# Kernel optimization log

Hardware: AMD Instinct MI355X
Metric: run time of the kernel (lower is better)

## Reference

```python
import jax, jax.numpy as jnp
import numpy as np

B, S, D, H = 2, 2048, 1024, 16
HD = D // H
NEG = -1000000.0


def setup_inputs() -> dict:
    key = jax.random.key(0)
    ks = jax.random.split(key, 8)
    sc = 1.0 / np.sqrt(D)
    return {
        "q": jax.random.normal(ks[0], (B, S, D), dtype=jnp.float32),
        "k": jax.random.normal(ks[1], (B, S, D), dtype=jnp.float32),
        "v": jax.random.normal(ks[2], (B, S, D), dtype=jnp.float32),
        "valid_lens": jax.random.randint(ks[3], (B,), 1, S + 1, dtype=jnp.int32),
        "Wq": jax.random.normal(ks[4], (D, D), dtype=jnp.float32) * sc,
        "Wk": jax.random.normal(ks[5], (D, D), dtype=jnp.float32) * sc,
        "Wv": jax.random.normal(ks[6], (D, D), dtype=jnp.float32) * sc,
        "Wo": jax.random.normal(ks[7], (D, D), dtype=jnp.float32) * sc,
    }


def reference(q, k, v, valid_lens, Wq, Wk, Wv, Wo):
    # projections: [B,S,D] -> [B,H,S,HD]
    def split_heads(x):
        return x.reshape(B, S, H, HD).transpose(0, 2, 1, 3)

    qh = split_heads(q @ Wq)
    kh = split_heads(k @ Wk)
    vh = split_heads(v @ Wv)

    # scaled dot-product scores: [B,H,Sq,Sk]
    scores = jnp.einsum("bhqd,bhkd->bhqk", qh, kh) / jnp.sqrt(
        jnp.asarray(HD, dtype=jnp.float32))

    # sequence mask over key axis: positions >= valid_len replaced by -1e6
    key_pos = jnp.arange(S, dtype=jnp.int32)
    mask = key_pos[None, :] < valid_lens[:, None]            # [B,Sk]
    scores = jnp.where(mask[:, None, None, :], scores, NEG)

    attn = jax.nn.softmax(scores, axis=-1)                   # dropout rate 0
    ctx = jnp.einsum("bhqk,bhkd->bhqd", attn, vh)            # [B,H,S,HD]
    out = ctx.transpose(0, 2, 1, 3).reshape(B, S, D)
    return out @ Wo
```

## Files before the change

### kernel.cpp

```cpp
#include <hip/hip_runtime.h>
#include <math.h>

#define NB 2
#define NS 2048
#define ND 1024
#define NH 16
#define NHD 64
#define GK 1024
#define NEG -1000000.0f

typedef __attribute__((ext_vector_type(4))) float f32x4;
typedef __attribute__((ext_vector_type(8))) _Float16 f16x8;
typedef __attribute__((ext_vector_type(4))) _Float16 f16x4;

typedef const __attribute__((address_space(1))) unsigned int* gas_t;
typedef __attribute__((address_space(3))) unsigned int* las_t;

__global__ __launch_bounds__(256) void wt_kernel(const float* __restrict__ Wq,
                                                 const float* __restrict__ Wk,
                                                 const float* __restrict__ Wv,
                                                 const float* __restrict__ Wo,
                                                 _Float16* __restrict__ WtBase) {
  __shared__ _Float16 Ts[64][72];
  const int which = blockIdx.x >> 8;
  const int rem = blockIdx.x & 255;
  const int tk = rem >> 4;
  const int tn = rem & 15;
  const float* W = which == 0 ? Wq : which == 1 ? Wk : which == 2 ? Wv : Wo;
  _Float16* Wt = WtBase + (size_t)which * (GK * ND);
  const int t = threadIdx.x;
#pragma unroll
  for (int p = 0; p < 4; ++p) {
    const int kr = (p << 4) + (t >> 4);
    const int nc = (t & 15) << 2;
    float4 v = *(const float4*)(W + (size_t)((tk << 6) + kr) * ND + (tn << 6) + nc);
    f16x4 h = {(_Float16)v.x, (_Float16)v.y, (_Float16)v.z, (_Float16)v.w};
    *(f16x4*)&Ts[kr][nc] = h;
  }
  __syncthreads();
#pragma unroll
  for (int p = 0; p < 4; ++p) {
    const int nr = (p << 4) + (t >> 4);
    const int kc = (t & 15) << 2;
    f16x4 h;
#pragma unroll
    for (int u = 0; u < 4; ++u) h[u] = Ts[kc + u][nr];
    *(f16x4*)(Wt + (size_t)((tn << 6) + nr) * GK + (tk << 6) + kc) = h;
  }
}

__global__ __launch_bounds__(256) void proj_kernel(const float* __restrict__ xq,
                                                   const float* __restrict__ xk,
                                                   const float* __restrict__ xv,
                                                   const _Float16* __restrict__ WtBase,
                                                   _Float16* __restrict__ Qh,
                                                   _Float16* __restrict__ Kh,
                                                   _Float16* __restrict__ VhT) {
  constexpr int BK = 32;
  __shared__ alignas(16) _Float16 As[128 * BK];
  __shared__ alignas(16) _Float16 Bs[128 * BK];

  int idx = ((blockIdx.x % 96) << 3) + (blockIdx.x / 96);
  const int which = idx >> 8;
  idx &= 255;
  const int bm = (idx >> 3) << 7;
  const int bn = (idx & 7) << 7;
  const float* A = which == 0 ? xq : which == 1 ? xk : xv;
  const _Float16* Bt = WtBase + (size_t)which * (ND * GK);

  const int tid = threadIdx.x, lane = tid & 63, w = tid >> 6;
  const int i16 = lane & 15, g4 = lane >> 4;
  const int wr = w >> 1, wc = w & 1;

  f32x4 acc[4][4] = {};

  for (int kt = 0; kt < GK / BK; ++kt) {
#pragma unroll
    for (int u = 0; u < 2; ++u) {
      const int c = (((w << 1) + u) << 6) + lane;
      const int r = c >> 2, sl = c & 3;
      const float* src = A + (size_t)(bm + r) * GK + (kt << 5) + ((sl ^ (r & 3)) << 3);
      float4 v0 = *(const float4*)src;
      float4 v1 = *(const float4*)(src + 4);
      f16x8 h;
#pragma unroll
      for (int j = 0; j < 4; ++j) { h[j] = (_Float16)v0[j]; h[4 + j] = (_Float16)v1[j]; }
      *(f16x8*)&As[(r << 5) + (sl << 3)] = h;
    }
#pragma unroll
    for (int u = 0; u < 2; ++u) {
      const int cb = ((w << 1) + u) << 6;
      const int c = cb + lane;
      const int r = c >> 2, sl = c & 3;
      __builtin_amdgcn_global_load_lds(
          (gas_t)(const void*)(Bt + (size_t)(bn + r) * GK + (kt << 5) + ((sl ^ (r & 3)) << 3)),
          (las_t)(void*)&Bs[cb << 3], 16, 0, 0);
    }
    __syncthreads();

    f16x8 af[4], bf[4];
#pragma unroll
    for (int mi = 0; mi < 4; ++mi) {
      const int r = (wr << 6) + (mi << 4) + i16;
      af[mi] = *(const f16x8*)&As[(r << 5) + ((g4 ^ (r & 3)) << 3)];
    }
#pragma unroll
    for (int ni = 0; ni < 4; ++ni) {
      const int r = (wc << 6) + (ni << 4) + i16;
      bf[ni] = *(const f16x8*)&Bs[(r << 5) + ((g4 ^ (r & 3)) << 3)];
    }
#pragma unroll
    for (int mi = 0; mi < 4; ++mi)
#pragma unroll
      for (int ni = 0; ni < 4; ++ni)
        acc[mi][ni] = __builtin_amdgcn_mfma_f32_16x16x32_f16(af[mi], bf[ni], acc[mi][ni], 0, 0, 0);
    __syncthreads();
  }

  if (which == 2) {
#pragma unroll
    for (int mi = 0; mi < 4; ++mi)
#pragma unroll
      for (int ni = 0; ni < 4; ++ni) {
        const int row0 = bm + (wr << 6) + (mi << 4) + (g4 << 2);
        const int col = bn + (wc << 6) + (ni << 4) + i16;
        const int bb = row0 >> 11, ss = row0 & (NS - 1);
        const int hh = col >> 6, dd = col & 63;
        f16x4 hv;
#pragma unroll
        for (int j = 0; j < 4; ++j) hv[j] = (_Float16)acc[mi][ni][j];
        *(f16x4*)&VhT[(((size_t)(bb * NH + hh) * NHD + dd) << 11) + ss] = hv;
      }
  } else {
    const float scale = which == 0 ? 0.125f : 1.0f;
    _Float16* Out = which == 0 ? Qh : Kh;
#pragma unroll
    for (int mi = 0; mi < 4; ++mi)
#pragma unroll
      for (int ni = 0; ni < 4; ++ni)
#pragma unroll
        for (int j = 0; j < 4; ++j) {
          const int row = bm + (wr << 6) + (mi << 4) + (g4 << 2) + j;
          const int col = bn + (wc << 6) + (ni << 4) + i16;
          const int bb = row >> 11, ss = row & (NS - 1);
          const int hh = col >> 6, dd = col & 63;
          Out[(((size_t)(bb * NH + hh) * NS + ss) << 6) + dd] = (_Float16)(acc[mi][ni][j] * scale);
        }
  }
}

__global__ __launch_bounds__(256) void attn_kernel(_Float16* __restrict__ Qc,
                                                   const _Float16* __restrict__ Kh,
                                                   const _Float16* __restrict__ VhT,
                                                   const int* __restrict__ valid_lens) {
  __shared__ alignas(16) _Float16 Ks[2][4096];
  __shared__ alignas(16) _Float16 Vt[2][4096];
  __shared__ alignas(16) _Float16 Ps[64][72];

  const int b0 = blockIdx.x;
  const int idx = ((b0 & 7) << 5) + ((b0 >> 8) << 8) + ((b0 >> 3) & 31);
  const int bh = idx >> 5, qt = idx & 31;
  const int valid = valid_lens[bh >> 4];
  const int tid = threadIdx.x, lane = tid & 63, w = tid >> 6;
  const int i16 = lane & 15, g4 = lane >> 4;

  _Float16* Qb = Qc + ((size_t)bh * NS + (qt << 6)) * NHD;
  const _Float16* Kb = Kh + (size_t)bh * NS * NHD;
  const _Float16* Vb = VhT + (size_t)bh * NHD * NS;

  f16x8 qf[2];
#pragma unroll
  for (int dc = 0; dc < 2; ++dc)
    qf[dc] = *(const f16x8*)(Qb + (size_t)((w << 4) + i16) * NHD + (dc << 5) + (g4 << 3));

  f32x4 acc[4] = {};
  float mrow[4] = {-1e30f, -1e30f, -1e30f, -1e30f};
  float lsum[4] = {0.f, 0.f, 0.f, 0.f};

  auto STAGE = [&](int buf, int t) {
#pragma unroll
    for (int u = 0; u < 2; ++u) {
      const int cb = ((w << 1) + u) << 6;
      const int c = cb + lane;
      const int r = c >> 3, sl = c & 7;
      const int so = (sl ^ (r & 7)) << 3;
      __builtin_amdgcn_global_load_lds(
          (gas_t)(const void*)(Kb + (size_t)((t << 6) + r) * NHD + so),
          (las_t)(void*)&Ks[buf][cb << 3], 16, 0, 0);
      __builtin_amdgcn_global_load_lds(
          (gas_t)(const void*)(Vb + (size_t)r * NS + (t << 6) + so),
          (las_t)(void*)&Vt[buf][cb << 3], 16, 0, 0);
    }
  };

  const int ntiles = (valid + 63) >> 6;
  STAGE(0, 0);

  for (int t = 0; t < ntiles; ++t) {
    __syncthreads();
    if (t + 1 < ntiles) STAGE((t + 1) & 1, t + 1);
    const int buf = t & 1;
    const bool full = ((t + 1) << 6) <= valid;

    float pj[4][4];
#pragma unroll
    for (int cf = 0; cf < 4; ++cf) {
      f32x4 sa = {};
      const int r = (cf << 4) + i16;
#pragma unroll
      for (int dc = 0; dc < 2; ++dc) {
        f16x8 kf = *(const f16x8*)&Ks[buf][(r << 6) + ((((dc << 2) + g4) ^ (r & 7)) << 3)];
        sa = __builtin_amdgcn_mfma_f32_16x16x32_f16(qf[dc], kf, sa, 0, 0, 0);
      }
      if (full) {
#pragma unroll
        for (int j = 0; j < 4; ++j) pj[cf][j] = sa[j];
      } else {
        const int kvcol = (t << 6) + r;
#pragma unroll
        for (int j = 0; j < 4; ++j) pj[cf][j] = (kvcol >= valid) ? NEG : sa[j];
      }
    }

    float tmax[4];
#pragma unroll
    for (int j = 0; j < 4; ++j)
      tmax[j] = fmaxf(fmaxf(pj[0][j], pj[1][j]), fmaxf(pj[2][j], pj[3][j]));
    for (int off = 1; off < 16; off <<= 1)
#pragma unroll
      for (int j = 0; j < 4; ++j)
        tmax[j] = fmaxf(tmax[j], __shfl_xor(tmax[j], off, 64));

    float rowsum[4] = {0.f, 0.f, 0.f, 0.f};
#pragma unroll
    for (int j = 0; j < 4; ++j) {
      const float mn = fmaxf(mrow[j], tmax[j]);
      const float scv = __expf(mrow[j] - mn);
      mrow[j] = mn;
      lsum[j] *= scv;
#pragma unroll
      for (int dn = 0; dn < 4; ++dn) acc[dn][j] *= scv;
    }
#pragma unroll
    for (int cf = 0; cf < 4; ++cf)
#pragma unroll
      for (int j = 0; j < 4; ++j) {
        const float p = __expf(pj[cf][j] - mrow[j]);
        rowsum[j] += p;
        Ps[(w << 4) + (g4 << 2) + j][(cf << 4) + i16] = (_Float16)p;
      }
    for (int off = 1; off < 16; off <<= 1)
#pragma unroll
      for (int j = 0; j < 4; ++j)
        rowsum[j] += __shfl_xor(rowsum[j], off, 64);
#pragma unroll
    for (int j = 0; j < 4; ++j) lsum[j] += rowsum[j];

#pragma unroll
    for (int ks = 0; ks < 2; ++ks) {
      f16x8 pf = *(const f16x8*)&Ps[(w << 4) + i16][(ks << 5) + (g4 << 3)];
#pragma unroll
      for (int dn = 0; dn < 4; ++dn) {
        const int d = (dn << 4) + i16;
        f16x8 vf = *(const f16x8*)&Vt[buf][(d << 6) + ((((ks << 2) + g4) ^ (d & 7)) << 3)];
        acc[dn] = __builtin_amdgcn_mfma_f32_16x16x32_f16(pf, vf, acc[dn], 0, 0, 0);
      }
    }
  }

#pragma unroll
  for (int dn = 0; dn < 4; ++dn)
#pragma unroll
    for (int j = 0; j < 4; ++j) {
      const int qrow = (w << 4) + (g4 << 2) + j;
      Qb[(size_t)qrow * NHD + (dn << 4) + i16] = (_Float16)(acc[dn][j] / lsum[j]);
    }
}

__global__ __launch_bounds__(256) void out_kernel(const _Float16* __restrict__ ctx,
                                                  const _Float16* __restrict__ Wot,
                                                  float* __restrict__ Out) {
  constexpr int BK = 32;
  __shared__ alignas(16) _Float16 As[128 * BK];
  __shared__ alignas(16) _Float16 Bs[64 * BK];

  const int idx = ((blockIdx.x % 64) << 3) + (blockIdx.x / 64);
  const int bm = (idx >> 4) << 7;
  const int bn = (idx & 15) << 6;

  const int tid = threadIdx.x, lane = tid & 63, w = tid >> 6;
  const int i16 = lane & 15, g4 = lane >> 4;
  const int wr = w >> 1, wc = w & 1;

  f32x4 acc[4][2] = {};

  for (int kt = 0; kt < GK / BK; ++kt) {
#pragma unroll
    for (int u = 0; u < 2; ++u) {
      const int cb = ((w << 1) + u) << 6;
      const int c = cb + lane;
      const int r = c >> 2, sl = c & 3;
      const int m = bm + r;
      const int kcol = (kt << 5) + ((sl ^ (r & 3)) << 3);
      const int bb = m >> 11, ss = m & (NS - 1);
      const int hh = kcol >> 6, dd = kcol & 63;
      __builtin_amdgcn_global_load_lds(
          (gas_t)(const void*)(ctx + (((size_t)(bb * NH + hh) * NS + ss) << 6) + dd),
          (las_t)(void*)&As[cb << 3], 16, 0, 0);
    }
    {
      const int cb = w << 6;
      const int c = cb + lane;
      const int r = c >> 2, sl = c & 3;
      __builtin_amdgcn_global_load_lds(
          (gas_t)(const void*)(Wot + (size_t)(bn + r) * GK + (kt << 5) + ((sl ^ (r & 3)) << 3)),
          (las_t)(void*)&Bs[cb << 3], 16, 0, 0);
    }
    __syncthreads();

    f16x8 af[4], bf[2];
#pragma unroll
    for (int mi = 0; mi < 4; ++mi) {
      const int r = (wr << 6) + (mi << 4) + i16;
      af[mi] = *(const f16x8*)&As[(r << 5) + ((g4 ^ (r & 3)) << 3)];
    }
#pragma unroll
    for (int ni = 0; ni < 2; ++ni) {
      const int r = (wc << 5) + (ni << 4) + i16;
      bf[ni] = *(const f16x8*)&Bs[(r << 5) + ((g4 ^ (r & 3)) << 3)];
    }
#pragma unroll
    for (int mi = 0; mi < 4; ++mi)
#pragma unroll
      for (int ni = 0; ni < 2; ++ni)
        acc[mi][ni] = __builtin_amdgcn_mfma_f32_16x16x32_f16(af[mi], bf[ni], acc[mi][ni], 0, 0, 0);
    __syncthreads();
  }

#pragma unroll
  for (int mi = 0; mi < 4; ++mi)
#pragma unroll
    for (int ni = 0; ni < 2; ++ni)
#pragma unroll
      for (int j = 0; j < 4; ++j) {
        const int row = bm + (wr << 6) + (mi << 4) + (g4 << 2) + j;
        const int col = bn + (wc << 5) + (ni << 4) + i16;
        Out[(size_t)row * ND + col] = acc[mi][ni][j];
      }
}

extern "C" void kernel_launch(void* const* d_in, const int* in_sizes, int n_in,
                              void* d_out, int out_size, void* d_ws, size_t ws_size,
                              hipStream_t stream) {
  const float* q  = (const float*)d_in[0];
  const float* k  = (const float*)d_in[1];
  const float* v  = (const float*)d_in[2];
  const int*   vl = (const int*)d_in[3];
  const float* Wq = (const float*)d_in[4];
  const float* Wk = (const float*)d_in[5];
  const float* Wv = (const float*)d_in[6];
  const float* Wo = (const float*)d_in[7];

  _Float16* ws = (_Float16*)d_ws;
  _Float16* Qh  = ws;
  _Float16* Kh  = ws + 4194304;
  _Float16* VhT = ws + 8388608;
  _Float16* Wt  = ws + 12582912;

  wt_kernel<<<dim3(1024), dim3(256), 0, stream>>>(Wq, Wk, Wv, Wo, Wt);
  proj_kernel<<<dim3(768), dim3(256), 0, stream>>>(q, k, v, Wt, Qh, Kh, VhT);
  attn_kernel<<<dim3(NB * NH * (NS >> 6)), dim3(256), 0, stream>>>(Qh, Kh, VhT, vl);
  out_kernel<<<dim3(512), dim3(256), 0, stream>>>(Qh, Wt + 3145728, (float*)d_out);
}
```

Measured before the change: 226.1 us.

## Pre-convert activations to fp16, split projection GEMMs, and streamline attention softmax

```diff
diff --git a/kernel.cpp b/kernel.cpp
--- a/kernel.cpp
+++ b/kernel.cpp
@@ -12,136 +12,162 @@
 typedef __attribute__((ext_vector_type(4))) float f32x4;
 typedef __attribute__((ext_vector_type(8))) _Float16 f16x8;
 typedef __attribute__((ext_vector_type(4))) _Float16 f16x4;
+typedef __attribute__((ext_vector_type(2))) __fp16 fp16x2_t;
 
 typedef const __attribute__((address_space(1))) unsigned int* gas_t;
 typedef __attribute__((address_space(3))) unsigned int* las_t;
 
-__global__ __launch_bounds__(256) void wt_kernel(const float* __restrict__ Wq,
-                                                 const float* __restrict__ Wk,
-                                                 const float* __restrict__ Wv,
-                                                 const float* __restrict__ Wo,
-                                                 _Float16* __restrict__ WtBase) {
-  __shared__ _Float16 Ts[64][72];
-  const int which = blockIdx.x >> 8;
-  const int rem = blockIdx.x & 255;
-  const int tk = rem >> 4;
-  const int tn = rem & 15;
-  const float* W = which == 0 ? Wq : which == 1 ? Wk : which == 2 ? Wv : Wo;
-  _Float16* Wt = WtBase + (size_t)which * (GK * ND);
-  const int t = threadIdx.x;
-#pragma unroll
-  for (int p = 0; p < 4; ++p) {
-    const int kr = (p << 4) + (t >> 4);
-    const int nc = (t & 15) << 2;
-    float4 v = *(const float4*)(W + (size_t)((tk << 6) + kr) * ND + (tn << 6) + nc);
-    f16x4 h = {(_Float16)v.x, (_Float16)v.y, (_Float16)v.z, (_Float16)v.w};
-    *(f16x4*)&Ts[kr][nc] = h;
-  }
-  __syncthreads();
-#pragma unroll
-  for (int p = 0; p < 4; ++p) {
-    const int nr = (p << 4) + (t >> 4);
-    const int kc = (t & 15) << 2;
-    f16x4 h;
-#pragma unroll
-    for (int u = 0; u < 4; ++u) h[u] = Ts[kc + u][nr];
-    *(f16x4*)(Wt + (size_t)((tn << 6) + nr) * GK + (tk << 6) + kc) = h;
-  }
-}
-
-__global__ __launch_bounds__(256) void proj_kernel(const float* __restrict__ xq,
+__global__ __launch_bounds__(256) void prep_kernel(const float* __restrict__ Wq,
+                                                   const float* __restrict__ Wk,
+                                                   const float* __restrict__ Wv,
+                                                   const float* __restrict__ Wo,
+                                                   const float* __restrict__ xq,
                                                    const float* __restrict__ xk,
                                                    const float* __restrict__ xv,
-                                                   const _Float16* __restrict__ WtBase,
-                                                   _Float16* __restrict__ Qh,
-                                                   _Float16* __restrict__ Kh,
-                                                   _Float16* __restrict__ VhT) {
-  constexpr int BK = 32;
-  __shared__ alignas(16) _Float16 As[128 * BK];
-  __shared__ alignas(16) _Float16 Bs[128 * BK];
-
-  int idx = ((blockIdx.x % 96) << 3) + (blockIdx.x / 96);
-  const int which = idx >> 8;
-  idx &= 255;
-  const int bm = (idx >> 3) << 7;
-  const int bn = (idx & 7) << 7;
-  const float* A = which == 0 ? xq : which == 1 ? xk : xv;
-  const _Float16* Bt = WtBase + (size_t)which * (ND * GK);
+                                                   _Float16* __restrict__ WtBase,
+                                                   _Float16* __restrict__ xhq,
+                                                   _Float16* __restrict__ xhk,
+                                                   _Float16* __restrict__ xhv) {
+  const int t = threadIdx.x;
+  if (blockIdx.x < 1024) {
+    __shared__ _Float16 Ts[64][72];
+    const int which = blockIdx.x >> 8;
+    const int rem = blockIdx.x & 255;
+    const int tk = rem >> 4;
+    const int tn = rem & 15;
+    const float* W = which == 0 ? Wq : which == 1 ? Wk : which == 2 ? Wv : Wo;
+    _Float16* Wt = WtBase + (size_t)which * (GK * ND);
+#pragma unroll
+    for (int p = 0; p < 4; ++p) {
+      const int kr = (p << 4) + (t >> 4);
+      const int nc = (t & 15) << 2;
+      float4 v = *(const float4*)(W + (size_t)((tk << 6) + kr) * ND + (tn << 6) + nc);
+      f16x4 h = {(_Float16)v.x, (_Float16)v.y, (_Float16)v.z, (_Float16)v.w};
+      *(f16x4*)&Ts[kr][nc] = h;
+    }
+    __syncthreads();
+#pragma unroll
+    for (int p = 0; p < 4; ++p) {
+      const int nr = (p << 4) + (t >> 4);
+      const int kc = (t & 15) << 2;
+      f16x4 h;
+#pragma unroll
+      for (int u = 0; u < 4; ++u) h[u] = Ts[kc + u][nr];
+      *(f16x4*)(Wt + (size_t)((tn << 6) + nr) * GK + (tk << 6) + kc) = h;
+    }
+  } else {
+    const int cid = blockIdx.x - 1024;
+    const int which = cid >> 11;
+    const float* src = which == 0 ? xq : which == 1 ? xk : xv;
+    _Float16* dst = which == 0 ? xhq : which == 1 ? xhk : xhv;
+    const size_t e0 = ((((size_t)(cid & 2047)) << 8) + t) << 3;
+    float4 v0 = *(const float4*)(src + e0);
+    float4 v1 = *(const float4*)(src + e0 + 4);
+    f16x8 h;
+#pragma unroll
+    for (int j = 0; j < 4; ++j) { h[j] = (_Float16)(&v0.x)[j]; h[4 + j] = (_Float16)(&v1.x)[j]; }
+    *(f16x8*)(dst + e0) = h;
+  }
+}
+
+template<int MODE>
+__global__ __launch_bounds__(256) void gemm16_kernel(const _Float16* __restrict__ A0,
+                                                     const _Float16* __restrict__ A1,
+                                                     const _Float16* __restrict__ Bt0,
+                                                     _Float16* __restrict__ O0,
+                                                     _Float16* __restrict__ O1) {
+  constexpr int BN = (MODE == 0) ? 128 : 64;
+  constexpr int NF = BN / 32;
+  __shared__ alignas(16) _Float16 As[128 * 32];
+  __shared__ alignas(16) _Float16 Bs[BN * 32];
+
+  const int b = blockIdx.x;
+  const int wg = ((b & 7) << 6) + (b >> 3);
+  int which, bm, bn;
+  if (MODE == 0) {
+    which = wg >> 8;
+    const int rem = wg & 255;
+    bm = (rem >> 3) << 7;
+    bn = (rem & 7) << 7;
+  } else {
+    which = 0;
+    bm = (wg >> 4) << 7;
+    bn = (wg & 15) << 6;
+  }
+  const _Float16* A = (MODE == 0 && which == 1) ? A1 : A0;
+  const _Float16* Bt = Bt0 + (size_t)which * (ND * GK);
 
   const int tid = threadIdx.x, lane = tid & 63, w = tid >> 6;
   const int i16 = lane & 15, g4 = lane >> 4;
   const int wr = w >> 1, wc = w & 1;
 
-  f32x4 acc[4][4] = {};
-
-  for (int kt = 0; kt < GK / BK; ++kt) {
-#pragma unroll
-    for (int u = 0; u < 2; ++u) {
-      const int c = (((w << 1) + u) << 6) + lane;
-      const int r = c >> 2, sl = c & 3;
-      const float* src = A + (size_t)(bm + r) * GK + (kt << 5) + ((sl ^ (r & 3)) << 3);
-      float4 v0 = *(const float4*)src;
-      float4 v1 = *(const float4*)(src + 4);
-      f16x8 h;
-#pragma unroll
-      for (int j = 0; j < 4; ++j) { h[j] = (_Float16)v0[j]; h[4 + j] = (_Float16)v1[j]; }
-      *(f16x8*)&As[(r << 5) + (sl << 3)] = h;
-    }
+  f32x4 acc[4][NF] = {};
+
+  for (int kt = 0; kt < GK / 32; ++kt) {
 #pragma unroll
     for (int u = 0; u < 2; ++u) {
       const int cb = ((w << 1) + u) << 6;
       const int c = cb + lane;
       const int r = c >> 2, sl = c & 3;
       __builtin_amdgcn_global_load_lds(
+          (gas_t)(const void*)(A + (size_t)(bm + r) * GK + (kt << 5) + ((sl ^ (r & 3)) << 3)),
+          (las_t)(void*)&As[cb << 3], 16, 0, 0);
+    }
+#pragma unroll
+    for (int u = 0; u < BN / 64; ++u) {
+      const int cb = ((w * (BN / 64)) + u) << 6;
+      const int c = cb + lane;
+      const int r = c >> 2, sl = c & 3;
+      __builtin_amdgcn_global_load_lds(
           (gas_t)(const void*)(Bt + (size_t)(bn + r) * GK + (kt << 5) + ((sl ^ (r & 3)) << 3)),
           (las_t)(void*)&Bs[cb << 3], 16, 0, 0);
     }
     __syncthreads();
 
-    f16x8 af[4], bf[4];
+    f16x8 af[4], bf[NF];
 #pragma unroll
     for (int mi = 0; mi < 4; ++mi) {
       const int r = (wr << 6) + (mi << 4) + i16;
       af[mi] = *(const f16x8*)&As[(r << 5) + ((g4 ^ (r & 3)) << 3)];
     }
 #pragma unroll
-    for (int ni = 0; ni < 4; ++ni) {
-      const int r = (wc << 6) + (ni << 4) + i16;
+    for (int ni = 0; ni < NF; ++ni) {
+      const int r = wc * (BN / 2) + (ni << 4) + i16;
       bf[ni] = *(const f16x8*)&Bs[(r << 5) + ((g4 ^ (r & 3)) << 3)];
     }
 #pragma unroll
     for (int mi = 0; mi < 4; ++mi)
 #pragma unroll
-      for (int ni = 0; ni < 4; ++ni)
+      for (int ni = 0; ni < NF; ++ni)
         acc[mi][ni] = __builtin_amdgcn_mfma_f32_16x16x32_f16(af[mi], bf[ni], acc[mi][ni], 0, 0, 0);
     __syncthreads();
   }
 
-  if (which == 2) {
+  if (MODE == 1) {
 #pragma unroll
     for (int mi = 0; mi < 4; ++mi)
 #pragma unroll
-      for (int ni = 0; ni < 4; ++ni) {
+      for (int ni = 0; ni < NF; ++ni) {
         const int row0 = bm + (wr << 6) + (mi << 4) + (g4 << 2);
-        const int col = bn + (wc << 6) + (ni << 4) + i16;
+        const int col = bn + wc * (BN / 2) + (ni << 4) + i16;
         const int bb = row0 >> 11, ss = row0 & (NS - 1);
         const int hh = col >> 6, dd = col & 63;
         f16x4 hv;
 #pragma unroll
         for (int j = 0; j < 4; ++j) hv[j] = (_Float16)acc[mi][ni][j];
-        *(f16x4*)&VhT[(((size_t)(bb * NH + hh) * NHD + dd) << 11) + ss] = hv;
+        *(f16x4*)&O0[(((size_t)(bb * NH + hh) * NHD + dd) << 11) + ss] = hv;
       }
   } else {
-    const float scale = which == 0 ? 0.125f : 1.0f;
-    _Float16* Out = which == 0 ? Qh : Kh;
+    const float scale = (which == 0) ? 0.125f : 1.0f;
+    _Float16* Out = (which == 0) ? O0 : O1;
 #pragma unroll
     for (int mi = 0; mi < 4; ++mi)
 #pragma unroll
-      for (int ni = 0; ni < 4; ++ni)
+      for (int ni = 0; ni < NF; ++ni)
 #pragma unroll
         for (int j = 0; j < 4; ++j) {
           const int row = bm + (wr << 6) + (mi << 4) + (g4 << 2) + j;
-          const int col = bn + (wc << 6) + (ni << 4) + i16;
+          const int col = bn + wc * (BN / 2) + (ni << 4) + i16;
           const int bb = row >> 11, ss = row & (NS - 1);
           const int hh = col >> 6, dd = col & 63;
           Out[(((size_t)(bb * NH + hh) * NS + ss) << 6) + dd] = (_Float16)(acc[mi][ni][j] * scale);
@@ -155,7 +181,7 @@
                                                    const int* __restrict__ valid_lens) {
   __shared__ alignas(16) _Float16 Ks[2][4096];
   __shared__ alignas(16) _Float16 Vt[2][4096];
-  __shared__ alignas(16) _Float16 Ps[64][72];
+  __shared__ alignas(16) unsigned int PsW[2048];
 
   const int b0 = blockIdx.x;
   const int idx = ((b0 & 7) << 5) + ((b0 >> 8) << 8) + ((b0 >> 3) & 31);
@@ -163,6 +189,7 @@
   const int valid = valid_lens[bh >> 4];
   const int tid = threadIdx.x, lane = tid & 63, w = tid >> 6;
   const int i16 = lane & 15, g4 = lane >> 4;
+  const int qrow = (w << 4) + i16;
 
   _Float16* Qb = Qc + ((size_t)bh * NS + (qt << 6)) * NHD;
   const _Float16* Kb = Kh + (size_t)bh * NS * NHD;
@@ -171,11 +198,11 @@
   f16x8 qf[2];
 #pragma unroll
   for (int dc = 0; dc < 2; ++dc)
-    qf[dc] = *(const f16x8*)(Qb + (size_t)((w << 4) + i16) * NHD + (dc << 5) + (g4 << 3));
+    qf[dc] = *(const f16x8*)(Qb + (size_t)qrow * NHD + (dc << 5) + (g4 << 3));
 
   f32x4 acc[4] = {};
-  float mrow[4] = {-1e30f, -1e30f, -1e30f, -1e30f};
-  float lsum[4] = {0.f, 0.f, 0.f, 0.f};
+  float mrow = -1e30f;
+  float lsum = 0.f;
 
   auto STAGE = [&](int buf, int t) {
 #pragma unroll
@@ -210,55 +237,63 @@
 #pragma unroll
       for (int dc = 0; dc < 2; ++dc) {
         f16x8 kf = *(const f16x8*)&Ks[buf][(r << 6) + ((((dc << 2) + g4) ^ (r & 7)) << 3)];
-        sa = __builtin_amdgcn_mfma_f32_16x16x32_f16(qf[dc], kf, sa, 0, 0, 0);
+        sa = __builtin_amdgcn_mfma_f32_16x16x32_f16(kf, qf[dc], sa, 0, 0, 0);
       }
       if (full) {
 #pragma unroll
         for (int j = 0; j < 4; ++j) pj[cf][j] = sa[j];
       } else {
-        const int kvcol = (t << 6) + r;
-#pragma unroll
-        for (int j = 0; j < 4; ++j) pj[cf][j] = (kvcol >= valid) ? NEG : sa[j];
-      }
-    }
-
-    float tmax[4];
-#pragma unroll
-    for (int j = 0; j < 4; ++j)
-      tmax[j] = fmaxf(fmaxf(pj[0][j], pj[1][j]), fmaxf(pj[2][j], pj[3][j]));
-    for (int off = 1; off < 16; off <<= 1)
-#pragma unroll
-      for (int j = 0; j < 4; ++j)
-        tmax[j] = fmaxf(tmax[j], __shfl_xor(tmax[j], off, 64));
-
-    float rowsum[4] = {0.f, 0.f, 0.f, 0.f};
-#pragma unroll
-    for (int j = 0; j < 4; ++j) {
-      const float mn = fmaxf(mrow[j], tmax[j]);
-      const float scv = __expf(mrow[j] - mn);
-      mrow[j] = mn;
-      lsum[j] *= scv;
-#pragma unroll
-      for (int dn = 0; dn < 4; ++dn) acc[dn][j] *= scv;
-    }
+        const int kvb = (t << 6) + (cf << 4) + (g4 << 2);
+#pragma unroll
+        for (int j = 0; j < 4; ++j) pj[cf][j] = (kvb + j >= valid) ? NEG : sa[j];
+      }
+    }
+
+    float m16 = pj[0][0];
 #pragma unroll
     for (int cf = 0; cf < 4; ++cf)
 #pragma unroll
+      for (int j = 0; j < 4; ++j) m16 = fmaxf(m16, pj[cf][j]);
+    m16 = fmaxf(m16, __shfl_xor(m16, 16, 64));
+    m16 = fmaxf(m16, __shfl_xor(m16, 32, 64));
+
+    if (__any(m16 > mrow + 8.0f)) {
+      const float mn = fmaxf(mrow, m16);
+      const float scv = __expf(mrow - mn);
+      mrow = mn;
+      lsum *= scv;
+#pragma unroll
       for (int j = 0; j < 4; ++j) {
-        const float p = __expf(pj[cf][j] - mrow[j]);
-        rowsum[j] += p;
-        Ps[(w << 4) + (g4 << 2) + j][(cf << 4) + i16] = (_Float16)p;
-      }
-    for (int off = 1; off < 16; off <<= 1)
-#pragma unroll
-      for (int j = 0; j < 4; ++j)
-        rowsum[j] += __shfl_xor(rowsum[j], off, 64);
-#pragma unroll
-    for (int j = 0; j < 4; ++j) lsum[j] += rowsum[j];
+        const float sj = __shfl(scv, (g4 << 2) + j, 64);
+#pragma unroll
+        for (int dn = 0; dn < 4; ++dn) acc[dn][j] *= sj;
+      }
+    }
+
+    float rsum = 0.f;
+#pragma unroll
+    for (int cf = 0; cf < 4; ++cf) {
+      float p0 = __expf(pj[cf][0] - mrow);
+      float p1 = __expf(pj[cf][1] - mrow);
+      float p2 = __expf(pj[cf][2] - mrow);
+      float p3 = __expf(pj[cf][3] - mrow);
+      rsum += (p0 + p1) + (p2 + p3);
+      union { fp16x2_t h; unsigned int u; } ca, cb2;
+      ca.h = __builtin_amdgcn_cvt_pkrtz(p0, p1);
+      cb2.h = __builtin_amdgcn_cvt_pkrtz(p2, p3);
+      const int u8 = (cf << 2) + g4;
+      const int s16 = (u8 >> 1) ^ (qrow & 7);
+      uint2 dv; dv.x = ca.u; dv.y = cb2.u;
+      *(uint2*)&PsW[(qrow << 5) + (s16 << 2) + ((u8 & 1) << 1)] = dv;
+    }
+    rsum += __shfl_xor(rsum, 16, 64);
+    rsum += __shfl_xor(rsum, 32, 64);
+    lsum += rsum;
 
 #pragma unroll
     for (int ks = 0; ks < 2; ++ks) {
-      f16x8 pf = *(const f16x8*)&Ps[(w << 4) + i16][(ks << 5) + (g4 << 3)];
+      const int cr = (ks << 2) + g4;
+      f16x8 pf = *(const f16x8*)&PsW[(qrow << 5) + ((cr ^ (qrow & 7)) << 2)];
 #pragma unroll
       for (int dn = 0; dn < 4; ++dn) {
         const int d = (dn << 4) + i16;
@@ -268,12 +303,16 @@
     }
   }
 
+  float linv[4];
+#pragma unroll
+  for (int j = 0; j < 4; ++j)
+    linv[j] = 1.0f / __shfl(lsum, (g4 << 2) + j, 64);
 #pragma unroll
   for (int dn = 0; dn < 4; ++dn)
 #pragma unroll
     for (int j = 0; j < 4; ++j) {
-      const int qrow = (w << 4) + (g4 << 2) + j;
-      Qb[(size_t)qrow * NHD + (dn << 4) + i16] = (_Float16)(acc[dn][j] / lsum[j]);
+      const int qr = (w << 4) + (g4 << 2) + j;
+      Qb[(size_t)qr * NHD + (dn << 4) + i16] = (_Float16)(acc[dn][j] * linv[j]);
     }
 }
 
@@ -367,8 +406,13 @@
   _Float16* VhT = ws + 8388608;
   _Float16* Wt  = ws + 12582912;
 
-  wt_kernel<<<dim3(1024), dim3(256), 0, stream>>>(Wq, Wk, Wv, Wo, Wt);
-  proj_kernel<<<dim3(768), dim3(256), 0, stream>>>(q, k, v, Wt, Qh, Kh, VhT);
+  _Float16* xhq = (_Float16*)d_out;
+  _Float16* xhk = xhq + 4194304;
+  _Float16* xhv = Qh;
+
+  prep_kernel<<<dim3(7168), dim3(256), 0, stream>>>(Wq, Wk, Wv, Wo, q, k, v, Wt, xhq, xhk, xhv);
+  gemm16_kernel<1><<<dim3(512), dim3(256), 0, stream>>>(xhv, xhv, Wt + 2097152, VhT, VhT);
+  gemm16_kernel<0><<<dim3(512), dim3(256), 0, stream>>>(xhq, xhk, Wt, Qh, Kh);
   attn_kernel<<<dim3(NB * NH * (NS >> 6)), dim3(256), 0, stream>>>(Qh, Kh, VhT, vl);
   out_kernel<<<dim3(512), dim3(256), 0, stream>>>(Qh, Wt + 3145728, (float*)d_out);
 }
```

Result: faster. 214.3 us (-5.2%).
